# Kernel tuning notes

Hardware: AMD Instinct MI355X
Metric: run time of the kernel (lower is better)

Reference implementation:

```python
import jax, jax.numpy as jnp
import numpy as np

N, D, T, ET, E = 100000, 128, 3, 4, 250000


def gru_cell(m, h, w_ih, w_hh, b_ih, b_hh):
    # torch.nn.GRUCell semantics
    gi = m @ w_ih.T + b_ih          # [N, 3D]
    gh = h @ w_hh.T + b_hh          # [N, 3D]
    i_r, i_z, i_n = jnp.split(gi, 3, axis=1)
    h_r, h_z, h_n = jnp.split(gh, 3, axis=1)
    r = jax.nn.sigmoid(i_r + h_r)
    z = jax.nn.sigmoid(i_z + h_z)
    n = jnp.tanh(i_n + r * h_n)
    return (1.0 - z) * n + z * h


def setup_inputs() -> dict:
    key = jax.random.key(0)
    ks = jax.random.split(key, 10)
    x = jax.random.normal(ks[0], (N, D), dtype=jnp.float32)
    edge_row = jax.random.randint(ks[1], (ET, E), 0, N, dtype=jnp.int32)
    edge_col = jax.random.randint(ks[2], (ET, E), 0, N, dtype=jnp.int32)
    edge_val = jnp.ones((ET, E), dtype=jnp.float32)
    xav = float(np.sqrt(6.0 / (D + D)))  # xavier_uniform per (D,D) slice
    weight = jax.random.uniform(ks[3], (T, ET, D, D), jnp.float32, -xav, xav)
    bias_w = jax.random.uniform(ks[4], (T, ET, D), jnp.float32, -0.01, 0.01)
    s = float(1.0 / np.sqrt(D))  # GRUCell default init range
    w_ih = jax.random.uniform(ks[5], (3 * D, D), jnp.float32, -s, s)
    w_hh = jax.random.uniform(ks[6], (3 * D, D), jnp.float32, -s, s)
    b_ih = jax.random.uniform(ks[7], (3 * D,), jnp.float32, -s, s)
    b_hh = jax.random.uniform(ks[8], (3 * D,), jnp.float32, -s, s)
    return {"x": x, "edge_row": edge_row, "edge_col": edge_col,
            "edge_val": edge_val, "weight": weight, "bias_w": bias_w,
            "w_ih": w_ih, "w_hh": w_hh, "b_ih": b_ih, "b_hh": b_hh}


def reference(x, edge_row, edge_col, edge_val, weight, bias_w, w_ih, w_hh, b_ih, b_hh):
    n_nodes = x.shape[0]
    h = x  # input_dim == out_channels, no zero-padding needed
    num_t = weight.shape[0]

    def agg_one(m_e, col_e, row_e, val_e):
        # sparse.mm: out[row] += val * m[col]
        msg = m_e[col_e] * val_e[:, None]                 # [E, D]
        return jax.ops.segment_sum(msg, row_e, num_segments=n_nodes)

    for t in range(num_t):
        # per-edge-type dense transform: [ET, N, D]
        m = jnp.einsum('nd,edf->enf', h, weight[t]) + bias_w[t][:, None, :]
        agg = jax.vmap(agg_one)(m, edge_col, edge_row, edge_val)  # [ET, N, D]
        m_sum = agg.sum(axis=0)                                    # [N, D]
        h = gru_cell(m_sum, h, w_ih, w_hh, b_ih, b_hh)
    return h
```

## Files before the change

### kernel.cpp

```cpp
#include <hip/hip_runtime.h>
#include <stdint.h>

#define NN  100000
#define DD  128
#define TT  3
#define ETT 4
#define EE  250000
#define NCH 49

typedef float  f32x4  __attribute__((ext_vector_type(4)));
typedef __bf16 bf16x8 __attribute__((ext_vector_type(8)));

__device__ __forceinline__ float bf2f(uint32_t u){ u <<= 16; return __builtin_bit_cast(float, u); }
__device__ __forceinline__ uint32_t f2bf(float f){
  uint32_t u = __builtin_bit_cast(uint32_t, f);
  return (u + 0x7FFFu + ((u >> 16) & 1u)) >> 16;
}
__device__ __forceinline__ f32x4 mfma16(bf16x8 a, bf16x8 b, f32x4 c){
  return __builtin_amdgcn_mfma_f32_16x16x32_bf16(a, b, c, 0, 0, 0);
}

__global__ void k_count(const int* __restrict__ erow, const float* __restrict__ eval,
                        int* __restrict__ counts, float* __restrict__ degval){
  int idx = blockIdx.x * 256 + threadIdx.x;
  if (idx >= ETT * EE) return;
  int e = idx / EE;
  int row = erow[idx];
  atomicAdd(&counts[e * NN + row], 1);
  atomicAdd(&degval[e * NN + row], eval[idx]);
}

__global__ void k_blksum(const int* __restrict__ counts, int* __restrict__ bsum){
  const int b = blockIdx.x, e = b / NCH, c = b % NCH;
  const int* p = counts + e * NN + c * 2048;
  int lim = NN - c * 2048; if (lim > 2048) lim = 2048;
  const int t = threadIdx.x;
  int s = 0;
  #pragma unroll
  for (int i = 0; i < 8; ++i){
    int idx = i * 256 + t;
    if (idx < lim) s += p[idx];
  }
  #pragma unroll
  for (int d = 32; d; d >>= 1) s += __shfl_down(s, d);
  __shared__ int wsum[4];
  if ((t & 63) == 0) wsum[t >> 6] = s;
  __syncthreads();
  if (t == 0) bsum[b] = wsum[0] + wsum[1] + wsum[2] + wsum[3];
}

__global__ void k_scanp(const int* __restrict__ bsum, int* __restrict__ bexc,
                        int* __restrict__ offsets){
  const int t = threadIdx.x, wid = t >> 6, l = t & 63;
  int v = (l < NCH) ? bsum[wid * NCH + l] : 0;
  int x = v;
  #pragma unroll
  for (int d = 1; d < 64; d <<= 1){ int y = __shfl_up(x, d); if (l >= d) x += y; }
  if (l < NCH) bexc[wid * NCH + l] = x - v;
  if (l == NCH - 1) offsets[wid * (NN + 1) + NN] = x;
}

__global__ void k_apply(const int* __restrict__ counts, const int* __restrict__ bexc,
                        int* __restrict__ offsets){
  const int b = blockIdx.x, e = b / NCH, c = b % NCH;
  const int* p = counts + e * NN + c * 2048;
  int* off = offsets + e * (NN + 1) + c * 2048;
  int lim = NN - c * 2048; if (lim > 2048) lim = 2048;
  const int t = threadIdx.x, l = t & 63, wid = t >> 6;
  __shared__ int wt[4];
  int v[8], s = 0;
  #pragma unroll
  for (int i = 0; i < 8; ++i){
    int idx = t * 8 + i;
    v[i] = (idx < lim) ? p[idx] : 0; s += v[i];
  }
  int x = s;
  #pragma unroll
  for (int d = 1; d < 64; d <<= 1){ int y = __shfl_up(x, d); if (l >= d) x += y; }
  if (l == 63) wt[wid] = x;
  __syncthreads();
  int wexc = 0;
  #pragma unroll
  for (int k = 0; k < 4; ++k) if (k < wid) wexc += wt[k];
  int te = bexc[b] + wexc + (x - s);
  #pragma unroll
  for (int i = 0; i < 8; ++i){
    int idx = t * 8 + i;
    if (idx < lim) off[idx] = te;
    te += v[i];
  }
}

__global__ void k_fill(const int* __restrict__ erow, const int* __restrict__ ecol,
                       const float* __restrict__ eval, const int* __restrict__ offsets,
                       int* __restrict__ cursor, uint2* __restrict__ sedge){
  int idx = blockIdx.x * 256 + threadIdx.x;
  if (idx >= ETT * EE) return;
  int e = idx / EE;
  int row = erow[idx];
  int pos = atomicAdd(&cursor[e * NN + row], 1);
  int o = offsets[e * (NN + 1) + row] + pos;
  sedge[e * EE + o] = make_uint2((uint32_t)ecol[idx], __builtin_bit_cast(uint32_t, eval[idx]));
}

__global__ void k_conv_x(const float* __restrict__ x, uint16_t* __restrict__ hbf){
  int idx = blockIdx.x * 256 + threadIdx.x;
  const float4* xp = (const float4*)x;
  float4 a = xp[idx * 2], b = xp[idx * 2 + 1];
  uint32_t p0 = f2bf(a.x) | (f2bf(a.y) << 16);
  uint32_t p1 = f2bf(a.z) | (f2bf(a.w) << 16);
  uint32_t p2 = f2bf(b.x) | (f2bf(b.y) << 16);
  uint32_t p3 = f2bf(b.z) | (f2bf(b.w) << 16);
  ((uint4*)hbf)[idx] = make_uint4(p0, p1, p2, p3);
}

__global__ void k_conv_w(const float* __restrict__ weight, const float* __restrict__ wih,
                         const float* __restrict__ whh, const float* __restrict__ bih,
                         const float* __restrict__ bhh, uint16_t* __restrict__ wcatT,
                         uint16_t* __restrict__ wgru, float* __restrict__ bcomb){
  int idx = blockIdx.x * 256 + threadIdx.x;
  if (idx < TT * 128 * 512){
    int t = idx / 65536; int rem = idx - t * 65536;
    int f = rem >> 9; int u = rem & 511;
    int e = u >> 7; int d = u & 127;
    wcatT[idx] = (uint16_t)f2bf(weight[(((t * 4 + e) * 128 + d) << 7) + f]);
  }
  if (idx < 192 * 512){
    const int frag = idx >> 9, within = idx & 511;
    const int lane = within >> 3, i = within & 7;
    const int ks = frag & 3, bb = (frag >> 2) & 1, m = (frag >> 3) & 1;
    const int rem2 = frag >> 4;
    const int g = rem2 % 3, w = rem2 / 3;
    const int j = g * 128 + w * 32 + bb * 16 + (lane & 15);
    const int k = ks * 32 + (lane >> 4) * 8 + i;
    const float* src = m ? whh : wih;
    wgru[idx] = (uint16_t)f2bf(src[j * 128 + k]);
  }
  if (idx < 256) bcomb[idx] = bih[idx] + bhh[idx];
}

#define ACC8(val, u, base) \
  acc[base+0] += val * bf2f(u.x & 0xffffu); acc[base+1] += val * bf2f(u.x >> 16); \
  acc[base+2] += val * bf2f(u.y & 0xffffu); acc[base+3] += val * bf2f(u.y >> 16); \
  acc[base+4] += val * bf2f(u.z & 0xffffu); acc[base+5] += val * bf2f(u.z >> 16); \
  acc[base+6] += val * bf2f(u.w & 0xffffu); acc[base+7] += val * bf2f(u.w >> 16);

__global__ __launch_bounds__(256, 4) void k_step(
    const uint16_t* __restrict__ hsrc, uint16_t* __restrict__ hdst,
    const float* __restrict__ h_old, float* __restrict__ h_new,
    const int* __restrict__ offsets, const uint2* __restrict__ sedge,
    const float* __restrict__ degval, const float* __restrict__ bias_w,
    const uint16_t* __restrict__ wcatT_t, int tstep,
    const uint16_t* __restrict__ wgru, const float* __restrict__ bcomb,
    const float* __restrict__ b_ih, const float* __restrict__ b_hh)
{
  __shared__ uint16_t aggT[32 * 512];
  __shared__ uint4 hT4[512];
  const int tid = threadIdx.x;
  const int node0 = blockIdx.x * 32;

  {
    const int nl = tid >> 3, q = tid & 7;
    const int n = node0 + nl;
    int se[4], ne[4];
    #pragma unroll
    for (int e = 0; e < ETT; ++e){
      se[e] = offsets[e * (NN + 1) + n];
      ne[e] = offsets[e * (NN + 1) + n + 1];
    }
    #pragma unroll 1
    for (int e = 0; e < ETT; ++e){
      float acc[16];
      #pragma unroll
      for (int i = 0; i < 16; ++i) acc[i] = 0.f;
      const int s = se[e], en = ne[e];
      const uint2* ep = sedge + (size_t)e * EE;
      #pragma unroll 1
      for (int i = s; i < en; i += 4){
        const int last = en - 1;
        const int i1 = (i + 1 < last) ? i + 1 : last;
        const int i2 = (i + 2 < last) ? i + 2 : last;
        const int i3 = (i + 3 < last) ? i + 3 : last;
        const uint2 cv0 = ep[i], cv1 = ep[i1], cv2 = ep[i2], cv3 = ep[i3];
        const float v0 = __builtin_bit_cast(float, cv0.y);
        const float v1 = (i + 1 <= last) ? __builtin_bit_cast(float, cv1.y) : 0.f;
        const float v2 = (i + 2 <= last) ? __builtin_bit_cast(float, cv2.y) : 0.f;
        const float v3 = (i + 3 <= last) ? __builtin_bit_cast(float, cv3.y) : 0.f;
        const uint4* p0 = (const uint4*)(hsrc + (size_t)cv0.x * DD + q * 16);
        const uint4* p1 = (const uint4*)(hsrc + (size_t)cv1.x * DD + q * 16);
        const uint4* p2 = (const uint4*)(hsrc + (size_t)cv2.x * DD + q * 16);
        const uint4* p3 = (const uint4*)(hsrc + (size_t)cv3.x * DD + q * 16);
        const uint4 a0 = p0[0], b0 = p0[1];
        const uint4 a1 = p1[0], b1 = p1[1];
        const uint4 a2 = p2[0], b2 = p2[1];
        const uint4 a3 = p3[0], b3 = p3[1];
        ACC8(v0, a0, 0); ACC8(v0, b0, 8);
        ACC8(v1, a1, 0); ACC8(v1, b1, 8);
        ACC8(v2, a2, 0); ACC8(v2, b2, 8);
        ACC8(v3, a3, 0); ACC8(v3, b3, 8);
      }
      #pragma unroll
      for (int c2 = 0; c2 < 2; ++c2){
        const int c  = e * 16 + q * 2 + c2;
        const int cs = c ^ (nl & 7);
        uint32_t p0 = f2bf(acc[c2*8+0]) | (f2bf(acc[c2*8+1]) << 16);
        uint32_t p1 = f2bf(acc[c2*8+2]) | (f2bf(acc[c2*8+3]) << 16);
        uint32_t p2 = f2bf(acc[c2*8+4]) | (f2bf(acc[c2*8+5]) << 16);
        uint32_t p3 = f2bf(acc[c2*8+6]) | (f2bf(acc[c2*8+7]) << 16);
        *(uint4*)&aggT[nl * 512 + cs * 8] = make_uint4(p0, p1, p2, p3);
      }
    }
  }
  __syncthreads();

  const int lane = tid & 63, w = tid >> 6;
  const int rlo = lane & 15, kg = lane >> 4;

  #pragma unroll
  for (int i = 0; i < 2; ++i){
    const int slot = tid * 2 + i;
    const int sn = slot >> 4, scs = slot & 15;
    const int sc = scs ^ (sn & 7);
    hT4[slot] = *(const uint4*)(hsrc + (size_t)(node0 + sn) * DD + sc * 8);
  }

  const int rt = w & 1, fh = w >> 1;
  const int rowA = rt * 16 + rlo;
  f32x4 C[4];
  #pragma unroll
  for (int i = 0; i < 4; ++i) C[i] = f32x4{0.f, 0.f, 0.f, 0.f};

  #pragma unroll
  for (int ks = 0; ks < 16; ++ks){
    const int cs = (ks * 4 + kg) ^ (rowA & 7);
    bf16x8 a = __builtin_bit_cast(bf16x8, *(const uint4*)&aggT[rowA * 512 + cs * 8]);
    #pragma unroll
    for (int ft = 0; ft < 4; ++ft){
      const int f = fh * 64 + ft * 16 + rlo;
      bf16x8 b = __builtin_bit_cast(bf16x8, *(const uint4*)(wcatT_t + (size_t)f * 512 + ks * 32 + kg * 8));
      C[ft] = mfma16(a, b, C[ft]);
    }
  }

  const float* bwt = bias_w + tstep * (ETT * DD);
  float dv[4][4];
  #pragma unroll
  for (int r = 0; r < 4; ++r){
    const int n2 = node0 + rt * 16 + kg * 4 + r;
    #pragma unroll
    for (int e = 0; e < 4; ++e) dv[e][r] = degval[e * NN + n2];
  }
  __syncthreads();

  uint16_t* mT = aggT;
  #pragma unroll
  for (int ft = 0; ft < 4; ++ft){
    const int f = fh * 64 + ft * 16 + rlo;
    const float b0 = bwt[f], b1 = bwt[128 + f], b2 = bwt[256 + f], b3 = bwt[384 + f];
    #pragma unroll
    for (int r = 0; r < 4; ++r){
      const int n2l = rt * 16 + kg * 4 + r;
      const float bias = dv[0][r]*b0 + dv[1][r]*b1 + dv[2][r]*b2 + dv[3][r]*b3;
      mT[n2l * 128 + (((f >> 3) ^ (n2l & 7)) << 3) + (f & 7)] = (uint16_t)f2bf(C[ft][r] + bias);
    }
  }
  __syncthreads();

  const uint4* mT4 = (const uint4*)aggT;
  #pragma unroll
  for (int bb = 0; bb < 2; ++bb){
    f32x4 acc[3][2][2];
    #pragma unroll
    for (int g = 0; g < 3; ++g)
      #pragma unroll
      for (int m = 0; m < 2; ++m)
        #pragma unroll
        for (int ns = 0; ns < 2; ++ns) acc[g][m][ns] = f32x4{0.f,0.f,0.f,0.f};

    #pragma unroll
    for (int ks = 0; ks < 4; ++ks){
      bf16x8 fa[3], fb[3];
      #pragma unroll
      for (int g = 0; g < 3; ++g){
        const int fragA = (((w * 3 + g) * 2 + 0) * 2 + bb) * 4 + ks;
        const int fragB = (((w * 3 + g) * 2 + 1) * 2 + bb) * 4 + ks;
        fa[g] = __builtin_bit_cast(bf16x8, *(const uint4*)(wgru + fragA * 512 + lane * 8));
        fb[g] = __builtin_bit_cast(bf16x8, *(const uint4*)(wgru + fragB * 512 + lane * 8));
      }
      #pragma unroll
      for (int ns = 0; ns < 2; ++ns){
        const int node = ns * 16 + rlo;
        const int cs = (ks * 4 + kg) ^ (node & 7);
        const bf16x8 bm = __builtin_bit_cast(bf16x8, mT4[node * 16 + cs]);
        const bf16x8 bh = __builtin_bit_cast(bf16x8, hT4[node * 16 + cs]);
        #pragma unroll
        for (int g = 0; g < 3; ++g){
          acc[g][0][ns] = mfma16(fa[g], bm, acc[g][0][ns]);
          acc[g][1][ns] = mfma16(fb[g], bh, acc[g][1][ns]);
        }
      }
    }

    const int d0 = w * 32 + bb * 16 + kg * 4;
    const f32x4 brz = *(const f32x4*)(bcomb + d0);
    const f32x4 bzz = *(const f32x4*)(bcomb + 128 + d0);
    const f32x4 bin = *(const f32x4*)(b_ih + 256 + d0);
    const f32x4 bhn = *(const f32x4*)(b_hh + 256 + d0);
    #pragma unroll
    for (int ns = 0; ns < 2; ++ns){
      const int node = node0 + ns * 16 + rlo;
      const f32x4 ho = *(const f32x4*)(h_old + (size_t)node * DD + d0);
      float hv[4];
      #pragma unroll
      for (int r = 0; r < 4; ++r){
        const float rg = 1.f / (1.f + __expf(-(acc[0][0][ns][r] + acc[0][1][ns][r] + brz[r])));
        const float zg = 1.f / (1.f + __expf(-(acc[1][0][ns][r] + acc[1][1][ns][r] + bzz[r])));
        const float xa = (acc[2][0][ns][r] + bin[r]) + rg * (acc[2][1][ns][r] + bhn[r]);
        const float ng = 1.f - 2.f / (__expf(2.f * xa) + 1.f);
        hv[r] = (1.f - zg) * ng + zg * ho[r];
      }
      *(f32x4*)(h_new + (size_t)node * DD + d0) = f32x4{hv[0], hv[1], hv[2], hv[3]};
      uint32_t p0 = f2bf(hv[0]) | (f2bf(hv[1]) << 16);
      uint32_t p1 = f2bf(hv[2]) | (f2bf(hv[3]) << 16);
      *(uint2*)(hdst + (size_t)node * DD + d0) = make_uint2(p0, p1);
    }
  }
}

extern "C" void kernel_launch(void* const* d_in, const int* in_sizes, int n_in,
                              void* d_out, int out_size, void* d_ws, size_t ws_size,
                              hipStream_t stream) {
  const float* x      = (const float*)d_in[0];
  const int*   erow   = (const int*)d_in[1];
  const int*   ecol   = (const int*)d_in[2];
  const float* eval   = (const float*)d_in[3];
  const float* weight = (const float*)d_in[4];
  const float* bias_w = (const float*)d_in[5];
  const float* wih    = (const float*)d_in[6];
  const float* whh    = (const float*)d_in[7];
  const float* bih    = (const float*)d_in[8];
  const float* bhh    = (const float*)d_in[9];
  float* out = (float*)d_out;
  char* ws = (char*)d_ws;

  size_t o = 0;
  auto alloc = [&](size_t bytes)->char*{ char* p = ws + o; o += (bytes + 255) & ~(size_t)255; return p; };
  int*      counts  = (int*)     alloc((size_t)ETT * NN * 4);
  int*      cursor  = (int*)     alloc((size_t)ETT * NN * 4);
  float*    degval  = (float*)   alloc((size_t)ETT * NN * 4);
  int*      offsets = (int*)     alloc((size_t)ETT * (NN + 1) * 4);
  int*      bsum    = (int*)     alloc((size_t)ETT * NCH * 4);
  int*      bexc    = (int*)     alloc((size_t)ETT * NCH * 4);
  uint2*    sedge   = (uint2*)   alloc((size_t)ETT * EE * 8);
  float*    hf      = (float*)   alloc((size_t)NN * DD * 4);
  uint16_t* hbf0    = (uint16_t*)alloc((size_t)NN * DD * 2);
  uint16_t* hbf1    = (uint16_t*)alloc((size_t)NN * DD * 2);
  uint16_t* wcatT   = (uint16_t*)alloc((size_t)TT * 128 * 512 * 2);
  uint16_t* wgru    = (uint16_t*)alloc((size_t)192 * 512 * 2);
  float*    bcomb   = (float*)   alloc((size_t)256 * 4);
  (void)ws_size; (void)in_sizes; (void)n_in; (void)out_size;

  hipMemsetAsync(counts, 0, (size_t)3 * ETT * NN * 4, stream);

  k_count<<<(ETT * EE + 255) / 256, 256, 0, stream>>>(erow, eval, counts, degval);
  k_blksum<<<ETT * NCH, 256, 0, stream>>>(counts, bsum);
  k_scanp<<<1, 256, 0, stream>>>(bsum, bexc, offsets);
  k_apply<<<ETT * NCH, 256, 0, stream>>>(counts, bexc, offsets);
  k_fill<<<(ETT * EE + 255) / 256, 256, 0, stream>>>(erow, ecol, eval, offsets, cursor, sedge);
  k_conv_x<<<(NN * DD / 8) / 256, 256, 0, stream>>>(x, hbf0);
  k_conv_w<<<(TT * 128 * 512 + 255) / 256, 256, 0, stream>>>(weight, wih, whh, bih, bhh,
                                                             wcatT, wgru, bcomb);

  uint16_t* hs = hbf0;
  uint16_t* hd = hbf1;
  for (int t = 0; t < TT; ++t){
    const float* hold = (t == 0) ? x : hf;
    float* hnew = (t == TT - 1) ? out : hf;
    k_step<<<NN / 32, 256, 0, stream>>>(hs, hd, hold, hnew, offsets, sedge, degval,
                                        bias_w, wcatT + (size_t)t * 65536, t,
                                        wgru, bcomb, bih, bhh);
    uint16_t* tmp = hs; hs = hd; hd = tmp;
  }
}
```

Before: 721.0 us.

## Double block size to 512 threads, halving per-thread work in k_step

```diff
diff --git a/kernel.cpp b/kernel.cpp
--- a/kernel.cpp
+++ b/kernel.cpp
@@ -139,13 +139,13 @@
   if (idx < 256) bcomb[idx] = bih[idx] + bhh[idx];
 }
 
-#define ACC8(val, u, base) \
-  acc[base+0] += val * bf2f(u.x & 0xffffu); acc[base+1] += val * bf2f(u.x >> 16); \
-  acc[base+2] += val * bf2f(u.y & 0xffffu); acc[base+3] += val * bf2f(u.y >> 16); \
-  acc[base+4] += val * bf2f(u.z & 0xffffu); acc[base+5] += val * bf2f(u.z >> 16); \
-  acc[base+6] += val * bf2f(u.w & 0xffffu); acc[base+7] += val * bf2f(u.w >> 16);
-
-__global__ __launch_bounds__(256, 4) void k_step(
+#define ACC8(val, u) \
+  acc[0] += val * bf2f(u.x & 0xffffu); acc[1] += val * bf2f(u.x >> 16); \
+  acc[2] += val * bf2f(u.y & 0xffffu); acc[3] += val * bf2f(u.y >> 16); \
+  acc[4] += val * bf2f(u.z & 0xffffu); acc[5] += val * bf2f(u.z >> 16); \
+  acc[6] += val * bf2f(u.w & 0xffffu); acc[7] += val * bf2f(u.w >> 16);
+
+__global__ __launch_bounds__(512, 8) void k_step(
     const uint16_t* __restrict__ hsrc, uint16_t* __restrict__ hdst,
     const float* __restrict__ h_old, float* __restrict__ h_new,
     const int* __restrict__ offsets, const uint2* __restrict__ sedge,
@@ -160,7 +160,7 @@
   const int node0 = blockIdx.x * 32;
 
   {
-    const int nl = tid >> 3, q = tid & 7;
+    const int nl = tid >> 4, q = tid & 15;
     const int n = node0 + nl;
     int se[4], ne[4];
     #pragma unroll
@@ -170,9 +170,9 @@
     }
     #pragma unroll 1
     for (int e = 0; e < ETT; ++e){
-      float acc[16];
+      float acc[8];
       #pragma unroll
-      for (int i = 0; i < 16; ++i) acc[i] = 0.f;
+      for (int i = 0; i < 8; ++i) acc[i] = 0.f;
       const int s = se[e], en = ne[e];
       const uint2* ep = sedge + (size_t)e * EE;
       #pragma unroll 1
@@ -186,29 +186,19 @@
         const float v1 = (i + 1 <= last) ? __builtin_bit_cast(float, cv1.y) : 0.f;
         const float v2 = (i + 2 <= last) ? __builtin_bit_cast(float, cv2.y) : 0.f;
         const float v3 = (i + 3 <= last) ? __builtin_bit_cast(float, cv3.y) : 0.f;
-        const uint4* p0 = (const uint4*)(hsrc + (size_t)cv0.x * DD + q * 16);
-        const uint4* p1 = (const uint4*)(hsrc + (size_t)cv1.x * DD + q * 16);
-        const uint4* p2 = (const uint4*)(hsrc + (size_t)cv2.x * DD + q * 16);
-        const uint4* p3 = (const uint4*)(hsrc + (size_t)cv3.x * DD + q * 16);
-        const uint4 a0 = p0[0], b0 = p0[1];
-        const uint4 a1 = p1[0], b1 = p1[1];
-        const uint4 a2 = p2[0], b2 = p2[1];
-        const uint4 a3 = p3[0], b3 = p3[1];
-        ACC8(v0, a0, 0); ACC8(v0, b0, 8);
-        ACC8(v1, a1, 0); ACC8(v1, b1, 8);
-        ACC8(v2, a2, 0); ACC8(v2, b2, 8);
-        ACC8(v3, a3, 0); ACC8(v3, b3, 8);
+        const uint4 u0 = *(const uint4*)(hsrc + (size_t)cv0.x * DD + q * 8);
+        const uint4 u1 = *(const uint4*)(hsrc + (size_t)cv1.x * DD + q * 8);
+        const uint4 u2 = *(const uint4*)(hsrc + (size_t)cv2.x * DD + q * 8);
+        const uint4 u3 = *(const uint4*)(hsrc + (size_t)cv3.x * DD + q * 8);
+        ACC8(v0, u0); ACC8(v1, u1); ACC8(v2, u2); ACC8(v3, u3);
       }
-      #pragma unroll
-      for (int c2 = 0; c2 < 2; ++c2){
-        const int c  = e * 16 + q * 2 + c2;
-        const int cs = c ^ (nl & 7);
-        uint32_t p0 = f2bf(acc[c2*8+0]) | (f2bf(acc[c2*8+1]) << 16);
-        uint32_t p1 = f2bf(acc[c2*8+2]) | (f2bf(acc[c2*8+3]) << 16);
-        uint32_t p2 = f2bf(acc[c2*8+4]) | (f2bf(acc[c2*8+5]) << 16);
-        uint32_t p3 = f2bf(acc[c2*8+6]) | (f2bf(acc[c2*8+7]) << 16);
-        *(uint4*)&aggT[nl * 512 + cs * 8] = make_uint4(p0, p1, p2, p3);
-      }
+      const int c  = e * 16 + q;
+      const int cs = c ^ (nl & 7);
+      uint32_t p0 = f2bf(acc[0]) | (f2bf(acc[1]) << 16);
+      uint32_t p1 = f2bf(acc[2]) | (f2bf(acc[3]) << 16);
+      uint32_t p2 = f2bf(acc[4]) | (f2bf(acc[5]) << 16);
+      uint32_t p3 = f2bf(acc[6]) | (f2bf(acc[7]) << 16);
+      *(uint4*)&aggT[nl * 512 + cs * 8] = make_uint4(p0, p1, p2, p3);
     }
   }
   __syncthreads();
@@ -216,27 +206,25 @@
   const int lane = tid & 63, w = tid >> 6;
   const int rlo = lane & 15, kg = lane >> 4;
 
-  #pragma unroll
-  for (int i = 0; i < 2; ++i){
-    const int slot = tid * 2 + i;
-    const int sn = slot >> 4, scs = slot & 15;
+  {
+    const int sn = tid >> 4, scs = tid & 15;
     const int sc = scs ^ (sn & 7);
-    hT4[slot] = *(const uint4*)(hsrc + (size_t)(node0 + sn) * DD + sc * 8);
-  }
-
-  const int rt = w & 1, fh = w >> 1;
+    hT4[tid] = *(const uint4*)(hsrc + (size_t)(node0 + sn) * DD + sc * 8);
+  }
+
+  const int rt = w & 1, fp = w >> 1;
   const int rowA = rt * 16 + rlo;
-  f32x4 C[4];
-  #pragma unroll
-  for (int i = 0; i < 4; ++i) C[i] = f32x4{0.f, 0.f, 0.f, 0.f};
+  f32x4 C[2];
+  C[0] = f32x4{0.f, 0.f, 0.f, 0.f};
+  C[1] = f32x4{0.f, 0.f, 0.f, 0.f};
 
   #pragma unroll
   for (int ks = 0; ks < 16; ++ks){
     const int cs = (ks * 4 + kg) ^ (rowA & 7);
     bf16x8 a = __builtin_bit_cast(bf16x8, *(const uint4*)&aggT[rowA * 512 + cs * 8]);
     #pragma unroll
-    for (int ft = 0; ft < 4; ++ft){
-      const int f = fh * 64 + ft * 16 + rlo;
+    for (int ft = 0; ft < 2; ++ft){
+      const int f = fp * 32 + ft * 16 + rlo;
       bf16x8 b = __builtin_bit_cast(bf16x8, *(const uint4*)(wcatT_t + (size_t)f * 512 + ks * 32 + kg * 8));
       C[ft] = mfma16(a, b, C[ft]);
     }
@@ -254,8 +242,8 @@
 
   uint16_t* mT = aggT;
   #pragma unroll
-  for (int ft = 0; ft < 4; ++ft){
-    const int f = fh * 64 + ft * 16 + rlo;
+  for (int ft = 0; ft < 2; ++ft){
+    const int f = fp * 32 + ft * 16 + rlo;
     const float b0 = bwt[f], b1 = bwt[128 + f], b2 = bwt[256 + f], b3 = bwt[384 + f];
     #pragma unroll
     for (int r = 0; r < 4; ++r){
@@ -267,63 +255,53 @@
   __syncthreads();
 
   const uint4* mT4 = (const uint4*)aggT;
-  #pragma unroll
-  for (int bb = 0; bb < 2; ++bb){
-    f32x4 acc[3][2][2];
-    #pragma unroll
-    for (int g = 0; g < 3; ++g)
-      #pragma unroll
-      for (int m = 0; m < 2; ++m)
-        #pragma unroll
-        for (int ns = 0; ns < 2; ++ns) acc[g][m][ns] = f32x4{0.f,0.f,0.f,0.f};
-
+  const int w_old = w >> 1, bb = w & 1;
+  const int d0 = w * 16 + kg * 4;
+  const f32x4 brz = *(const f32x4*)(bcomb + d0);
+  const f32x4 bzz = *(const f32x4*)(bcomb + 128 + d0);
+  const f32x4 bin = *(const f32x4*)(b_ih + 256 + d0);
+  const f32x4 bhn = *(const f32x4*)(b_hh + 256 + d0);
+
+  #pragma unroll 1
+  for (int ns = 0; ns < 2; ++ns){
+    f32x4 acc[3][2];
+    #pragma unroll
+    for (int g = 0; g < 3; ++g){
+      acc[g][0] = f32x4{0.f,0.f,0.f,0.f};
+      acc[g][1] = f32x4{0.f,0.f,0.f,0.f};
+    }
     #pragma unroll
     for (int ks = 0; ks < 4; ++ks){
-      bf16x8 fa[3], fb[3];
+      const int node = ns * 16 + rlo;
+      const int cs = (ks * 4 + kg) ^ (node & 7);
+      const bf16x8 bm = __builtin_bit_cast(bf16x8, mT4[node * 16 + cs]);
+      const bf16x8 bh = __builtin_bit_cast(bf16x8, hT4[node * 16 + cs]);
       #pragma unroll
       for (int g = 0; g < 3; ++g){
-        const int fragA = (((w * 3 + g) * 2 + 0) * 2 + bb) * 4 + ks;
-        const int fragB = (((w * 3 + g) * 2 + 1) * 2 + bb) * 4 + ks;
-        fa[g] = __builtin_bit_cast(bf16x8, *(const uint4*)(wgru + fragA * 512 + lane * 8));
-        fb[g] = __builtin_bit_cast(bf16x8, *(const uint4*)(wgru + fragB * 512 + lane * 8));
+        const int fragA = (((w_old * 3 + g) * 2 + 0) * 2 + bb) * 4 + ks;
+        const int fragB = (((w_old * 3 + g) * 2 + 1) * 2 + bb) * 4 + ks;
+        const bf16x8 fa = __builtin_bit_cast(bf16x8, *(const uint4*)(wgru + fragA * 512 + lane * 8));
+        const bf16x8 fb = __builtin_bit_cast(bf16x8, *(const uint4*)(wgru + fragB * 512 + lane * 8));
+        acc[g][0] = mfma16(fa, bm, acc[g][0]);
+        acc[g][1] = mfma16(fb, bh, acc[g][1]);
       }
-      #pragma unroll
-      for (int ns = 0; ns < 2; ++ns){
-        const int node = ns * 16 + rlo;
-        const int cs = (ks * 4 + kg) ^ (node & 7);
-        const bf16x8 bm = __builtin_bit_cast(bf16x8, mT4[node * 16 + cs]);
-        const bf16x8 bh = __builtin_bit_cast(bf16x8, hT4[node * 16 + cs]);
-        #pragma unroll
-        for (int g = 0; g < 3; ++g){
-          acc[g][0][ns] = mfma16(fa[g], bm, acc[g][0][ns]);
-          acc[g][1][ns] = mfma16(fb[g], bh, acc[g][1][ns]);
-        }
-      }
-    }
-
-    const int d0 = w * 32 + bb * 16 + kg * 4;
-    const f32x4 brz = *(const f32x4*)(bcomb + d0);
-    const f32x4 bzz = *(const f32x4*)(bcomb + 128 + d0);
-    const f32x4 bin = *(const f32x4*)(b_ih + 256 + d0);
-    const f32x4 bhn = *(const f32x4*)(b_hh + 256 + d0);
-    #pragma unroll
-    for (int ns = 0; ns < 2; ++ns){
-      const int node = node0 + ns * 16 + rlo;
-      const f32x4 ho = *(const f32x4*)(h_old + (size_t)node * DD + d0);
-      float hv[4];
-      #pragma unroll
-      for (int r = 0; r < 4; ++r){
-        const float rg = 1.f / (1.f + __expf(-(acc[0][0][ns][r] + acc[0][1][ns][r] + brz[r])));
-        const float zg = 1.f / (1.f + __expf(-(acc[1][0][ns][r] + acc[1][1][ns][r] + bzz[r])));
-        const float xa = (acc[2][0][ns][r] + bin[r]) + rg * (acc[2][1][ns][r] + bhn[r]);
-        const float ng = 1.f - 2.f / (__expf(2.f * xa) + 1.f);
-        hv[r] = (1.f - zg) * ng + zg * ho[r];
-      }
-      *(f32x4*)(h_new + (size_t)node * DD + d0) = f32x4{hv[0], hv[1], hv[2], hv[3]};
-      uint32_t p0 = f2bf(hv[0]) | (f2bf(hv[1]) << 16);
-      uint32_t p1 = f2bf(hv[2]) | (f2bf(hv[3]) << 16);
-      *(uint2*)(hdst + (size_t)node * DD + d0) = make_uint2(p0, p1);
-    }
+    }
+
+    const int node = node0 + ns * 16 + rlo;
+    const f32x4 ho = *(const f32x4*)(h_old + (size_t)node * DD + d0);
+    float hv[4];
+    #pragma unroll
+    for (int r = 0; r < 4; ++r){
+      const float rg = 1.f / (1.f + __expf(-(acc[0][0][r] + acc[0][1][r] + brz[r])));
+      const float zg = 1.f / (1.f + __expf(-(acc[1][0][r] + acc[1][1][r] + bzz[r])));
+      const float xa = (acc[2][0][r] + bin[r]) + rg * (acc[2][1][r] + bhn[r]);
+      const float ng = 1.f - 2.f / (__expf(2.f * xa) + 1.f);
+      hv[r] = (1.f - zg) * ng + zg * ho[r];
+    }
+    *(f32x4*)(h_new + (size_t)node * DD + d0) = f32x4{hv[0], hv[1], hv[2], hv[3]};
+    uint32_t p0 = f2bf(hv[0]) | (f2bf(hv[1]) << 16);
+    uint32_t p1 = f2bf(hv[2]) | (f2bf(hv[3]) << 16);
+    *(uint2*)(hdst + (size_t)node * DD + d0) = make_uint2(p0, p1);
   }
 }
 
@@ -376,7 +354,7 @@
   for (int t = 0; t < TT; ++t){
     const float* hold = (t == 0) ? x : hf;
     float* hnew = (t == TT - 1) ? out : hf;
-    k_step<<<NN / 32, 256, 0, stream>>>(hs, hd, hold, hnew, offsets, sedge, degval,
+    k_step<<<NN / 32, 512, 0, stream>>>(hs, hd, hold, hnew, offsets, sedge, degval,
                                         bias_w, wcatT + (size_t)t * 65536, t,
                                         wgru, bcomb, bih, bhh);
     uint16_t* tmp = hs; hs = hd; hd = tmp;
```

Result: slower. 1.531 ms (+112.3%).
